# Optimization experiments

Measured on AMD Instinct MI355X. Metric: run time of the kernel, lower is better.

The kernel has to match this reference:

```python
import math
import jax, jax.numpy as jnp
import numpy as np

S, B, H = 2048, 1, 4096
NH, HD = 32, 128          # heads, head dim
ROT = HD // 2             # rotary dim per 2D-RoPE half = 64


def rotate_half(x):
    x1, x2 = jnp.split(x, 2, axis=-1)
    return jnp.concatenate([-x2, x1], axis=-1)


def rope_tables(seq_len, dim, base=10000.0):
    inv_freq = 1.0 / (base ** (jnp.arange(0, dim, 2, dtype=jnp.float32) / dim))
    freqs = jnp.arange(seq_len, dtype=jnp.float32)[:, None] * inv_freq[None, :]
    emb = jnp.concatenate([freqs, freqs], axis=-1)  # [S, dim]
    return jnp.cos(emb), jnp.sin(emb)


def apply_rope(q, k, cos, sin, pos):
    # q,k: [S,B,NH,ROT]; pos: [S,B] -> gather cos/sin per token
    c = cos[pos][:, :, None, :]  # [S,B,1,ROT]
    s = sin[pos][:, :, None, :]
    return q * c + rotate_half(q) * s, k * c + rotate_half(k) * s


def setup_inputs() -> dict:
    key = jax.random.key(0)
    ks = jax.random.split(key, 5)
    hidden_states = jax.random.normal(ks[0], (S, B, H), dtype=jnp.float32)
    pos = jnp.arange(S, dtype=jnp.int64 if jax.config.jax_enable_x64 else jnp.int32)
    position_ids = jnp.stack([pos, pos])[None]  # [B=1, 2, S]
    attention_mask = jnp.triu(jnp.ones((S, S), dtype=bool), k=1)[None, None]  # True = masked
    scale = 0.02
    wqkv = jax.random.normal(ks[1], (3 * H, H), dtype=jnp.float32) * scale
    bqkv = jax.random.normal(ks[2], (3 * H,), dtype=jnp.float32) * scale
    wdense = jax.random.normal(ks[3], (H, H), dtype=jnp.float32) * scale
    bdense = jax.random.normal(ks[4], (H,), dtype=jnp.float32) * scale
    return {"hidden_states": hidden_states, "position_ids": position_ids,
            "attention_mask": attention_mask, "wqkv": wqkv, "bqkv": bqkv,
            "wdense": wdense, "bdense": bdense, "layer_id": 1}


def reference(hidden_states, position_ids, attention_mask, wqkv, bqkv, wdense, bdense, layer_id):
    s, b, h = hidden_states.shape
    # fused QKV projection: [S,B,NH,3*HD]
    mixed = (jnp.einsum('sbh,oh->sbo', hidden_states, wqkv) + bqkv).reshape(s, b, NH, 3 * HD)
    q, k, v = jnp.split(mixed, 3, axis=-1)  # each [S,B,NH,HD]

    # 2D RoPE: split head dim in half, rotate each half with its own position ids
    q1, q2 = jnp.split(q, 2, axis=-1)
    k1, k2 = jnp.split(k, 2, axis=-1)
    cos, sin = rope_tables(s, ROT)
    pos = position_ids[:, 0, :].T       # [S,B]
    block_pos = position_ids[:, 1, :].T  # [S,B]
    q1, k1 = apply_rope(q1, k1, cos, sin, pos)
    q2, k2 = apply_rope(q2, k2, cos, sin, block_pos)
    q = jnp.concatenate([q1, q2], axis=-1)
    k = jnp.concatenate([k1, k2], axis=-1)

    # layer-scaled attention (ChatGLM style)
    coeff = float(layer_id + 1)
    q = q / (math.sqrt(HD) * coeff)
    scores = jnp.einsum('sbhd,tbhd->bhst', q, k)  # [B,NH,S,S]
    scores = jnp.where(attention_mask, jnp.float32(-10000.0), scores)
    scores = scores.astype(jnp.float32) * coeff
    probs = jax.nn.softmax(scores, axis=-1).astype(q.dtype)
    context = jnp.einsum('bhst,tbhd->sbhd', probs, v).reshape(s, b, h)

    out = jnp.einsum('sbh,oh->sbo', context, wdense) + bdense
    return out
```

## Files before the change

kernel.cpp:

```cpp
#include <hip/hip_runtime.h>

typedef unsigned short u16;
typedef unsigned int u32;
typedef __attribute__((ext_vector_type(4))) float f32x4;
typedef __attribute__((ext_vector_type(16))) float f32x16;
typedef __attribute__((ext_vector_type(8))) short bf16x8;
typedef __attribute__((ext_vector_type(2))) unsigned int u32x2;

#define S_LEN 2048
#define NHEAD 32
#define HDD 128
#define HID 4096
#define N_QKV 12288
#define KDIM 4096
#define RS 12288

__device__ __forceinline__ u16 f2bf(float f) {
  u32 u = __builtin_bit_cast(u32, f);
  u = (u + 0x7FFFu + ((u >> 16) & 1u)) >> 16;
  return (u16)u;
}
__device__ __forceinline__ float bf2f(u16 h) {
  u32 u = ((u32)h) << 16;
  return __builtin_bit_cast(float, u);
}

__device__ __forceinline__ void gl2lds16(const void* g, void* l) {
  __builtin_amdgcn_global_load_lds(
      (const __attribute__((address_space(1))) u32*)g,
      (__attribute__((address_space(3))) u32*)l, 16, 0, 0);
}

#define FULL_BAR()                          \
  {                                         \
    asm volatile("" ::: "memory");          \
    __builtin_amdgcn_s_barrier();           \
    asm volatile("" ::: "memory");          \
  }

__global__ __launch_bounds__(256) void cvt3_kernel(const float* __restrict__ s0, u16* __restrict__ d0, int n0,
                                                   const float* __restrict__ s2, u16* __restrict__ d2, int n2,
                                                   float* __restrict__ cos_t, float* __restrict__ sin_t) {
  int i = blockIdx.x * blockDim.x + threadIdx.x;
  if (i < S_LEN * 32) {
    int s = i >> 5, ii = i & 31;
    float invf = expf(-0.28782313662425572f * (float)ii);
    float a = (float)s * invf;
    cos_t[i] = cosf(a);
    sin_t[i] = sinf(a);
  }
  int st = gridDim.x * blockDim.x;
  int ntot = n0 + n2;
  for (; i < ntot; i += st) {
    const float* s;
    u16* d;
    int j = i;
    if (j < n0) {
      s = s0; d = d0;
    } else {
      j -= n0; s = s2; d = d2;
    }
    float4 v = ((const float4*)s)[j];
    u32x2 o;
    o.x = (u32)f2bf(v.x) | ((u32)f2bf(v.y) << 16);
    o.y = (u32)f2bf(v.z) | ((u32)f2bf(v.w) << 16);
    ((u32x2*)d)[j] = o;
  }
}

__global__ __launch_bounds__(256) void ropek_kernel(u16* __restrict__ mixed,
                                                    const int* __restrict__ pid,
                                                    const float* __restrict__ cos_t,
                                                    const float* __restrict__ sin_t) {
  int idx = blockIdx.x * blockDim.x + threadIdx.x;
  const int total = NHEAD * S_LEN * 2 * 8;
  if (idx >= total) return;
  int j = idx & 7;
  int half = (idx >> 3) & 1;
  int s = (idx >> 4) & (S_LEN - 1);
  int h = idx >> 15;
  int i0 = j * 4;
  int p = pid[half * S_LEN + s];
  float4 c4 = *(const float4*)(cos_t + p * 32 + i0);
  float4 s4 = *(const float4*)(sin_t + p * 32 + i0);
  u16* base = mixed + (size_t)s * RS + h * 384 + 128 + half * 64 + i0;
  ushort4 x1v = *(const ushort4*)(base);
  ushort4 x2v = *(const ushort4*)(base + 32);
  ushort4 o1, o2;
  {
    float x1 = bf2f(x1v.x), x2 = bf2f(x2v.x);
    o1.x = f2bf(x1 * c4.x - x2 * s4.x);
    o2.x = f2bf(x2 * c4.x + x1 * s4.x);
  }
  {
    float x1 = bf2f(x1v.y), x2 = bf2f(x2v.y);
    o1.y = f2bf(x1 * c4.y - x2 * s4.y);
    o2.y = f2bf(x2 * c4.y + x1 * s4.y);
  }
  {
    float x1 = bf2f(x1v.z), x2 = bf2f(x2v.z);
    o1.z = f2bf(x1 * c4.z - x2 * s4.z);
    o2.z = f2bf(x2 * c4.z + x1 * s4.z);
  }
  {
    float x1 = bf2f(x1v.w), x2 = bf2f(x2v.w);
    o1.w = f2bf(x1 * c4.w - x2 * s4.w);
    o2.w = f2bf(x2 * c4.w + x1 * s4.w);
  }
  *(ushort4*)(base) = o1;
  *(ushort4*)(base + 32) = o2;
}

__global__ __launch_bounds__(512, 2) void gemmQ(const u16* __restrict__ A,
                                                const u16* __restrict__ B,
                                                const float* __restrict__ bias,
                                                u16* __restrict__ outb) {
  __shared__ __align__(16) char lds[3][40960];

  const int tid = threadIdx.x;
  const int lane = tid & 63, w = tid >> 6;
  const int l31 = lane & 31, hh = lane >> 5;
  const int wm = w >> 2, wn = w & 3;

  int x = blockIdx.x & 7, loc = blockIdx.x >> 3;
  int mb = loc & 7, nb = x * 4 + (loc >> 3);
  const int bm = mb * 256, bn = nb * 384;

  f32x16 acc[4][3];
#pragma unroll
  for (int mi = 0; mi < 4; ++mi)
#pragma unroll
    for (int ni = 0; ni < 3; ++ni)
#pragma unroll
      for (int r = 0; r < 16; ++r) acc[mi][ni][r] = 0.f;

  const size_t K2 = (size_t)KDIM * 2;

  const char* gA[2];
#pragma unroll
  for (int j = 0; j < 2; ++j) {
    int slot = j * 512 + tid;
    int line = slot >> 3;
    int sl = (slot & 7) ^ (line & 7);
    int row = 2 * line + (sl >> 2);
    int colb = (sl & 3) * 16;
    gA[j] = (const char*)A + (size_t)(bm + row) * K2 + colb;
  }
  const char* gB[3];
#pragma unroll
  for (int j = 0; j < 3; ++j) {
    int slot = j * 512 + tid;
    int line = slot >> 3;
    int sl = (slot & 7) ^ (line & 7);
    int row = 2 * line + (sl >> 2);
    int colb = (sl & 3) * 16;
    gB[j] = (const char*)B + (size_t)(bn + row) * K2 + colb;
  }
  const int ldst = w * 1024;

#define QIA(t, bi)                                                  \
  {                                                                 \
    char* Lb = lds[bi];                                             \
    gl2lds16(gA[0] + (size_t)(t) * 64, Lb + ldst);                  \
    gl2lds16(gA[1] + (size_t)(t) * 64, Lb + 8192 + ldst);           \
  }
#define QIB(t, bi)                                                  \
  {                                                                 \
    char* Lb = lds[bi] + 16384;                                     \
    _Pragma("unroll")                                               \
    for (int j = 0; j < 3; ++j)                                     \
      gl2lds16(gB[j] + (size_t)(t) * 64, Lb + j * 8192 + ldst);     \
  }

  int offA[4][2], offB[3][2];
#pragma unroll
  for (int mi = 0; mi < 4; ++mi) {
    int r = wm * 128 + mi * 32 + l31;
    int line = r >> 1;
#pragma unroll
    for (int kk = 0; kk < 2; ++kk) {
      int sl = (((r & 1) << 2) + kk * 2 + hh) ^ (line & 7);
      offA[mi][kk] = line * 128 + sl * 16;
    }
  }
#pragma unroll
  for (int ni = 0; ni < 3; ++ni) {
    int r = wn * 96 + ni * 32 + l31;
    int line = r >> 1;
#pragma unroll
    for (int kk = 0; kk < 2; ++kk) {
      int sl = (((r & 1) << 2) + kk * 2 + hh) ^ (line & 7);
      offB[ni][kk] = 16384 + line * 128 + sl * 16;
    }
  }

  QIA(0, 0); QIB(0, 0);
  QIA(1, 1); QIB(1, 1);
  asm volatile("s_waitcnt vmcnt(5)" ::: "memory");
  FULL_BAR();

  int cur = 0, nx2 = 2;
  for (int kt = 0; kt < 128; ++kt) {
    const char* buf = lds[cur];
    const bool pf = (kt + 2) < 128;
    bf16x8 a[4], b[3];
#pragma unroll
    for (int mi = 0; mi < 4; ++mi) a[mi] = *(const bf16x8*)(buf + offA[mi][0]);
#pragma unroll
    for (int ni = 0; ni < 3; ++ni) b[ni] = *(const bf16x8*)(buf + offB[ni][0]);
    if (pf) QIA(kt + 2, nx2);
    FULL_BAR();
    __builtin_amdgcn_s_setprio(1);
#pragma unroll
    for (int mi = 0; mi < 4; ++mi)
#pragma unroll
      for (int ni = 0; ni < 3; ++ni)
        acc[mi][ni] = __builtin_amdgcn_mfma_f32_32x32x16_bf16(a[mi], b[ni], acc[mi][ni], 0, 0, 0);
    __builtin_amdgcn_s_setprio(0);
#pragma unroll
    for (int mi = 0; mi < 4; ++mi) a[mi] = *(const bf16x8*)(buf + offA[mi][1]);
#pragma unroll
    for (int ni = 0; ni < 3; ++ni) b[ni] = *(const bf16x8*)(buf + offB[ni][1]);
    if (pf) {
      QIB(kt + 2, nx2);
      asm volatile("s_waitcnt vmcnt(5)" ::: "memory");
    } else if (kt == 126) {
      asm volatile("s_waitcnt vmcnt(0)" ::: "memory");
    }
    FULL_BAR();
    __builtin_amdgcn_s_setprio(1);
#pragma unroll
    for (int mi = 0; mi < 4; ++mi)
#pragma unroll
      for (int ni = 0; ni < 3; ++ni)
        acc[mi][ni] = __builtin_amdgcn_mfma_f32_32x32x16_bf16(a[mi], b[ni], acc[mi][ni], 0, 0, 0);
    __builtin_amdgcn_s_setprio(0);
    cur = (cur + 1 == 3) ? 0 : cur + 1;
    nx2 = (nx2 + 1 == 3) ? 0 : nx2 + 1;
  }
#undef QIA
#undef QIB

#pragma unroll
  for (int ni = 0; ni < 3; ++ni) {
    int n = bn + wn * 96 + ni * 32 + l31;
    float bv = bias[n];
#pragma unroll
    for (int mi = 0; mi < 4; ++mi) {
      int m0 = bm + wm * 128 + mi * 32 + 4 * hh;
#pragma unroll
      for (int reg = 0; reg < 16; ++reg) {
        int row = m0 + (reg & 3) + 8 * (reg >> 2);
        outb[(size_t)row * N_QKV + n] = f2bf(acc[mi][ni][reg] + bv);
      }
    }
  }
}

__global__ __launch_bounds__(512, 2) void gemmD(const u16* __restrict__ A,
                                                const float* __restrict__ Bf,
                                                const float* __restrict__ bias,
                                                float* __restrict__ outf) {
  __shared__ __align__(16) char lds[2][49152];

  const int tid = threadIdx.x;
  const int lane = tid & 63, w = tid >> 6;
  const int l15 = lane & 15, g = lane >> 4;
  const int wm = w >> 1, wn = w & 1;

  int x = blockIdx.x & 7, loc = blockIdx.x >> 3;
  int mb = loc & 7, nb = x * 4 + (loc >> 3);
  const int bm = mb * 256, bn = nb * 128;

  f32x4 acc[4][4];
  f32x4 z4 = {0.f, 0.f, 0.f, 0.f};
#pragma unroll
  for (int mi = 0; mi < 4; ++mi)
#pragma unroll
    for (int ni = 0; ni < 4; ++ni) acc[mi][ni] = z4;

  const size_t K2 = (size_t)KDIM * 2;

  const char* gA[2];
#pragma unroll
  for (int j = 0; j < 2; ++j) {
    int slot = j * 512 + tid;
    int line = slot >> 3;
    int sl = (slot & 7) ^ (line & 7);
    int row = 2 * line + (sl >> 2);
    int colb = (sl & 3) * 16;
    gA[j] = (const char*)A + (size_t)(bm + row) * K2 + colb;
  }
  int bline = tid >> 3;
  int bsl = tid & 7;
  int brow = 2 * bline + (bsl >> 2);
  int bcole = (bsl & 3) * 8;
  const float* gBs = Bf + (size_t)(bn + brow) * KDIM + bcole;
  int bphys = bsl ^ (bline & 7);
  const int bwr = 32768 + bline * 128 + bphys * 16;
  const int ldst = w * 1024;

#define DIA(t, kk)                                                            \
  {                                                                           \
    char* Lb = lds[(t) & 1] + (kk) * 16384;                                   \
    gl2lds16(gA[0] + (size_t)(t) * 128 + (kk) * 64, Lb + ldst);               \
    gl2lds16(gA[1] + (size_t)(t) * 128 + (kk) * 64, Lb + 8192 + ldst);        \
  }
#define DGB(t)                                                                \
  {                                                                           \
    const float* p0 = gBs + (size_t)(t) * 64;                                 \
    b0a = *(const float4*)(p0);                                               \
    b0b = *(const float4*)(p0 + 4);                                           \
    b1a = *(const float4*)(p0 + 32);                                          \
    b1b = *(const float4*)(p0 + 36);                                          \
  }
#define DWB(t)                                                                \
  {                                                                           \
    bf16x8 o0, o1;                                                            \
    o0[0] = (short)f2bf(b0a.x); o0[1] = (short)f2bf(b0a.y);                   \
    o0[2] = (short)f2bf(b0a.z); o0[3] = (short)f2bf(b0a.w);                   \
    o0[4] = (short)f2bf(b0b.x); o0[5] = (short)f2bf(b0b.y);                   \
    o0[6] = (short)f2bf(b0b.z); o0[7] = (short)f2bf(b0b.w);                   \
    o1[0] = (short)f2bf(b1a.x); o1[1] = (short)f2bf(b1a.y);                   \
    o1[2] = (short)f2bf(b1a.z); o1[3] = (short)f2bf(b1a.w);                   \
    o1[4] = (short)f2bf(b1b.x); o1[5] = (short)f2bf(b1b.y);                   \
    o1[6] = (short)f2bf(b1b.z); o1[7] = (short)f2bf(b1b.w);                   \
    char* Lb = lds[(t) & 1];                                                  \
    *(bf16x8*)(Lb + bwr) = o0;                                                \
    *(bf16x8*)(Lb + 8192 + bwr) = o1;                                         \
  }

  int offA[4], offB[2][4];
#pragma unroll
  for (int mi = 0; mi < 4; ++mi) {
    int r = wm * 64 + mi * 16 + l15;
    int line = r >> 1;
    int sl = (((r & 1) << 2) + g) ^ (line & 7);
    offA[mi] = line * 128 + sl * 16;
  }
#pragma unroll
  for (int kk = 0; kk < 2; ++kk)
#pragma unroll
    for (int ni = 0; ni < 4; ++ni) {
      int r = wn * 64 + ni * 16 + l15;
      int line = r >> 1;
      int sl = (((r & 1) << 2) + g) ^ (line & 7);
      offB[kk][ni] = 32768 + kk * 8192 + line * 128 + sl * 16;
    }

  float4 b0a, b0b, b1a, b1b;
  DGB(0);
  DIA(0, 0);
  DIA(0, 1);
  asm volatile("s_waitcnt vmcnt(4)" ::: "memory");
  DWB(0);
  asm volatile("s_waitcnt vmcnt(0) lgkmcnt(0)" ::: "memory");
  FULL_BAR();

  for (int kt = 0; kt < 64; ++kt) {
    const char* buf = lds[kt & 1];
    const bool pf = (kt + 1) < 64;
    bf16x8 a[4], b[4];
#pragma unroll
    for (int mi = 0; mi < 4; ++mi) a[mi] = *(const bf16x8*)(buf + offA[mi]);
#pragma unroll
    for (int ni = 0; ni < 4; ++ni) b[ni] = *(const bf16x8*)(buf + offB[0][ni]);
    if (pf) {
      DIA(kt + 1, 0);
      DGB(kt + 1);
      asm volatile("s_waitcnt vmcnt(6)" ::: "memory");
    } else {
      asm volatile("s_waitcnt vmcnt(0)" ::: "memory");
    }
    FULL_BAR();
    __builtin_amdgcn_s_setprio(1);
#pragma unroll
    for (int mi = 0; mi < 4; ++mi)
#pragma unroll
      for (int ni = 0; ni < 4; ++ni)
        acc[mi][ni] = __builtin_amdgcn_mfma_f32_16x16x32_bf16(a[mi], b[ni], acc[mi][ni], 0, 0, 0);
    __builtin_amdgcn_s_setprio(0);
#pragma unroll
    for (int mi = 0; mi < 4; ++mi) a[mi] = *(const bf16x8*)(buf + 16384 + offA[mi]);
#pragma unroll
    for (int ni = 0; ni < 4; ++ni) b[ni] = *(const bf16x8*)(buf + offB[1][ni]);
    if (pf) {
      DIA(kt + 1, 1);
      asm volatile("s_waitcnt vmcnt(2)" ::: "memory");
      DWB(kt + 1);
      asm volatile("s_waitcnt lgkmcnt(0)" ::: "memory");
    }
    FULL_BAR();
    __builtin_amdgcn_s_setprio(1);
#pragma unroll
    for (int mi = 0; mi < 4; ++mi)
#pragma unroll
      for (int ni = 0; ni < 4; ++ni)
        acc[mi][ni] = __builtin_amdgcn_mfma_f32_16x16x32_bf16(a[mi], b[ni], acc[mi][ni], 0, 0, 0);
    __builtin_amdgcn_s_setprio(0);
  }
#undef DIA
#undef DGB
#undef DWB

#pragma unroll
  for (int ni = 0; ni < 4; ++ni) {
    int n = bn + wn * 64 + ni * 16 + l15;
    float bv = bias[n];
#pragma unroll
    for (int mi = 0; mi < 4; ++mi) {
      int m0 = bm + wm * 64 + mi * 16 + 4 * g;
#pragma unroll
      for (int rr = 0; rr < 4; ++rr) outf[(size_t)(m0 + rr) * HID + n] = acc[mi][ni][rr] + bv;
    }
  }
}

__global__ __launch_bounds__(256) void attn_kernel(const u16* __restrict__ mixed,
                                                   const int* __restrict__ pid,
                                                   const float* __restrict__ cos_t,
                                                   const float* __restrict__ sin_t,
                                                   u16* __restrict__ ctx) {
  __shared__ __align__(16) u16 Ksh[64 * 136];
  __shared__ __align__(16) u16 Vsh[128 * 64];
  __shared__ __align__(16) u16 Pt[4][16 * 72];

  int tid = threadIdx.x;
  int lane = tid & 63, w = tid >> 6;
  int lane15 = lane & 15, g = lane >> 4;

  int bpair = blockIdx.x & 15;
  int h = blockIdx.x >> 4;

  const u16* qp = mixed + (size_t)h * 384;
  const u16* kp = mixed + (size_t)h * 384 + 128;
  const u16* vp = mixed + (size_t)h * 384 + 256;

  int krow = tid >> 2, kc = (tid & 3) * 32;
  int vk0 = 2 * (tid & 31), vd0 = (tid >> 5) * 16;
  f32x4 z4 = {0.f, 0.f, 0.f, 0.f};
  const float QSC = 0.08838834764831845f;
  const float L2E = 1.4426950408889634f;

  for (int pass = 0; pass < 2; ++pass) {
    int qi = pass ? (31 - bpair) : bpair;
    int qbase = qi * 64;
    int qrow = qbase + w * 16 + lane15;
    int ntiles = qi + 1;

    bf16x8 qf[4];
    const u16* qptr = qp + (size_t)qrow * RS + g * 8;
#pragma unroll
    for (int d0 = 0; d0 < 4; ++d0) qf[d0] = *(const bf16x8*)(qptr + d0 * 32);
    {
      int p1 = pid[qrow], p2 = pid[S_LEN + qrow];
      float cc[8], ss[8], dd[8], tt[8];
#pragma unroll
      for (int j = 0; j < 8; ++j) {
        cc[j] = cos_t[p1 * 32 + g * 8 + j];
        ss[j] = sin_t[p1 * 32 + g * 8 + j];
        dd[j] = cos_t[p2 * 32 + g * 8 + j];
        tt[j] = sin_t[p2 * 32 + g * 8 + j];
      }
#pragma unroll
      for (int j = 0; j < 8; ++j) {
        float x1 = bf2f((u16)qf[0][j]), x2 = bf2f((u16)qf[1][j]);
        qf[0][j] = (short)f2bf((x1 * cc[j] - x2 * ss[j]) * QSC);
        qf[1][j] = (short)f2bf((x2 * cc[j] + x1 * ss[j]) * QSC);
        float y1 = bf2f((u16)qf[2][j]), y2 = bf2f((u16)qf[3][j]);
        qf[2][j] = (short)f2bf((y1 * dd[j] - y2 * tt[j]) * QSC);
        qf[3][j] = (short)f2bf((y2 * dd[j] + y1 * tt[j]) * QSC);
      }
    }

    f32x4 pv[8];
#pragma unroll
    for (int db = 0; db < 8; ++db) pv[db] = z4;
    float m_run = -1e30f, l_run = 0.0f;

    for (int t = 0; t < ntiles; ++t) {
      int kb0 = t * 64;
      __syncthreads();
      {
        const bf16x8* src = (const bf16x8*)(kp + (size_t)(kb0 + krow) * RS + kc);
#pragma unroll
        for (int c = 0; c < 4; ++c)
          *(bf16x8*)(Ksh + krow * 136 + kc + c * 8) = src[c];
        const bf16x8* r0p = (const bf16x8*)(vp + (size_t)(kb0 + vk0) * RS + vd0);
        const bf16x8* r1p = (const bf16x8*)(vp + (size_t)(kb0 + vk0 + 1) * RS + vd0);
        bf16x8 r00 = r0p[0], r01 = r0p[1];
        bf16x8 r10 = r1p[0], r11 = r1p[1];
#pragma unroll
        for (int jj = 0; jj < 8; ++jj) {
          int d = vd0 + jj;
          u32 v0 = (u32)(u16)r00[jj] | ((u32)(u16)r10[jj] << 16);
          *(u32*)((char*)Vsh + d * 128 + (((vk0 >> 3) ^ (d & 7)) << 4) + (vk0 & 7) * 2) = v0;
          int d2 = vd0 + 8 + jj;
          u32 v1 = (u32)(u16)r01[jj] | ((u32)(u16)r11[jj] << 16);
          *(u32*)((char*)Vsh + d2 * 128 + (((vk0 >> 3) ^ (d2 & 7)) << 4) + (vk0 & 7) * 2) = v1;
        }
      }
      __syncthreads();

      f32x4 sa[4];
#pragma unroll
      for (int kt16 = 0; kt16 < 4; ++kt16) sa[kt16] = z4;
#pragma unroll
      for (int kt16 = 0; kt16 < 4; ++kt16)
#pragma unroll
        for (int d0 = 0; d0 < 4; ++d0) {
          bf16x8 kf = *(const bf16x8*)(Ksh + (kt16 * 16 + lane15) * 136 + d0 * 32 + g * 8);
          sa[kt16] = __builtin_amdgcn_mfma_f32_16x16x32_bf16(kf, qf[d0], sa[kt16], 0, 0, 0);
        }
      float s[16];
#pragma unroll
      for (int kt16 = 0; kt16 < 4; ++kt16)
#pragma unroll
        for (int rr = 0; rr < 4; ++rr) {
          int kg = kb0 + kt16 * 16 + 4 * g + rr;
          s[kt16 * 4 + rr] = (kg > qrow) ? -1e30f : sa[kt16][rr];
        }
      float mx = s[0];
#pragma unroll
      for (int i2 = 1; i2 < 16; ++i2) mx = fmaxf(mx, s[i2]);
      mx = fmaxf(mx, __shfl_xor(mx, 16));
      mx = fmaxf(mx, __shfl_xor(mx, 32));
      float mnew = fmaxf(m_run, mx);
      float fac = exp2f((m_run - mnew) * L2E);
      float p[16], psum = 0.f;
#pragma unroll
      for (int i2 = 0; i2 < 16; ++i2) {
        p[i2] = exp2f((s[i2] - mnew) * L2E);
        psum += p[i2];
      }
      psum += __shfl_xor(psum, 16);
      psum += __shfl_xor(psum, 32);
      l_run = l_run * fac + psum;
      m_run = mnew;
#pragma unroll
      for (int db = 0; db < 8; ++db) pv[db] *= fac;

#pragma unroll
      for (int kt16 = 0; kt16 < 4; ++kt16) {
        u32x2 pw;
        pw.x = (u32)f2bf(p[kt16 * 4 + 0]) | ((u32)f2bf(p[kt16 * 4 + 1]) << 16);
        pw.y = (u32)f2bf(p[kt16 * 4 + 2]) | ((u32)f2bf(p[kt16 * 4 + 3]) << 16);
        *(u32x2*)(&Pt[w][lane15 * 72 + kt16 * 16 + 4 * g]) = pw;
      }
      asm volatile("s_waitcnt lgkmcnt(0)" ::: "memory");
      bf16x8 pf0 = *(const bf16x8*)(&Pt[w][lane15 * 72 + 8 * g]);
      bf16x8 pf1 = *(const bf16x8*)(&Pt[w][lane15 * 72 + 32 + 8 * g]);

#pragma unroll
      for (int db = 0; db < 8; ++db) {
        int d = db * 16 + lane15;
        bf16x8 vf0 = *(const bf16x8*)((const char*)Vsh + d * 128 + ((g ^ (d & 7)) << 4));
        bf16x8 vf1 = *(const bf16x8*)((const char*)Vsh + d * 128 + (((4 + g) ^ (d & 7)) << 4));
        pv[db] = __builtin_amdgcn_mfma_f32_16x16x32_bf16(vf0, pf0, pv[db], 0, 0, 0);
        pv[db] = __builtin_amdgcn_mfma_f32_16x16x32_bf16(vf1, pf1, pv[db], 0, 0, 0);
      }
    }

    float inv = 1.0f / l_run;
#pragma unroll
    for (int db = 0; db < 8; ++db) {
      ushort4 o;
      o.x = f2bf(pv[db][0] * inv);
      o.y = f2bf(pv[db][1] * inv);
      o.z = f2bf(pv[db][2] * inv);
      o.w = f2bf(pv[db][3] * inv);
      *(ushort4*)(ctx + (size_t)qrow * HID + h * HDD + db * 16 + 4 * g) = o;
    }
    __syncthreads();
  }
}

extern "C" void kernel_launch(void* const* d_in, const int* in_sizes, int n_in,
                              void* d_out, int out_size, void* d_ws, size_t ws_size,
                              hipStream_t stream) {
  const float* hidden = (const float*)d_in[0];
  const int* pid = (const int*)d_in[1];
  const float* wqkv = (const float*)d_in[3];
  const float* bqkv = (const float*)d_in[4];
  const float* wdense = (const float*)d_in[5];
  const float* bdense = (const float*)d_in[6];
  float* out = (float*)d_out;

  char* ws = (char*)d_ws;
  u16* W1 = (u16*)ws;
  u16* X = (u16*)(ws + 134217728);
  u16* mixed = (u16*)(ws + 150994944);
  u16* ctx = (u16*)(ws + 201326592);
  float* cos_t = (float*)(ws + 218103808);
  float* sin_t = (float*)(ws + 218365952);

  cvt3_kernel<<<dim3(2048), dim3(256), 0, stream>>>(
      wqkv, W1, N_QKV * KDIM / 4, hidden, X, S_LEN * HID / 4, cos_t, sin_t);

  gemmQ<<<dim3(256), dim3(512), 0, stream>>>(X, W1, bqkv, mixed);

  ropek_kernel<<<dim3(4096), dim3(256), 0, stream>>>(mixed, pid, cos_t, sin_t);

  attn_kernel<<<dim3(512), dim3(256), 0, stream>>>(mixed, pid, cos_t, sin_t, ctx);

  gemmD<<<dim3(256), dim3(512), 0, stream>>>(ctx, wdense, bdense, out);
}
```

Measured before the change: 484.9 us.

## Switch dense-projection GEMM to 32x32x16 MFMA and change LDS swizzle key

The output-projection GEMM now uses 32x32x16 bf16 MFMA tiles (2x2 per wave) instead of 16x16x32 (4x4 per wave), with LDS fragment offsets and the epilogue row mapping rewritten to match. The LDS XOR swizzle key in both GEMMs changes from line&7 to (line^(line>>1))&7, aiming to cut bank conflicts on the fragment reads. Larger MFMA tiles mean fewer instructions and fewer LDS reads per flop, but they carry different latency and register pressure, and the swizzle change alters the global-to-LDS load address pattern.

```diff
diff --git a/kernel.cpp b/kernel.cpp
--- a/kernel.cpp
+++ b/kernel.cpp
@@ -24,6 +24,8 @@
   u32 u = ((u32)h) << 16;
   return __builtin_bit_cast(float, u);
 }
+
+__device__ __forceinline__ int gkey(int line) { return (line ^ (line >> 1)) & 7; }
 
 __device__ __forceinline__ void gl2lds16(const void* g, void* l) {
   __builtin_amdgcn_global_load_lds(
@@ -141,7 +143,7 @@
   for (int j = 0; j < 2; ++j) {
     int slot = j * 512 + tid;
     int line = slot >> 3;
-    int sl = (slot & 7) ^ (line & 7);
+    int sl = (slot & 7) ^ gkey(line);
     int row = 2 * line + (sl >> 2);
     int colb = (sl & 3) * 16;
     gA[j] = (const char*)A + (size_t)(bm + row) * K2 + colb;
@@ -151,7 +153,7 @@
   for (int j = 0; j < 3; ++j) {
     int slot = j * 512 + tid;
     int line = slot >> 3;
-    int sl = (slot & 7) ^ (line & 7);
+    int sl = (slot & 7) ^ gkey(line);
     int row = 2 * line + (sl >> 2);
     int colb = (sl & 3) * 16;
     gB[j] = (const char*)B + (size_t)(bn + row) * K2 + colb;
@@ -179,7 +181,7 @@
     int line = r >> 1;
 #pragma unroll
     for (int kk = 0; kk < 2; ++kk) {
-      int sl = (((r & 1) << 2) + kk * 2 + hh) ^ (line & 7);
+      int sl = (((r & 1) << 2) + kk * 2 + hh) ^ gkey(line);
       offA[mi][kk] = line * 128 + sl * 16;
     }
   }
@@ -189,7 +191,7 @@
     int line = r >> 1;
 #pragma unroll
     for (int kk = 0; kk < 2; ++kk) {
-      int sl = (((r & 1) << 2) + kk * 2 + hh) ^ (line & 7);
+      int sl = (((r & 1) << 2) + kk * 2 + hh) ^ gkey(line);
       offB[ni][kk] = 16384 + line * 128 + sl * 16;
     }
   }
@@ -265,19 +267,20 @@
 
   const int tid = threadIdx.x;
   const int lane = tid & 63, w = tid >> 6;
-  const int l15 = lane & 15, g = lane >> 4;
+  const int l31 = lane & 31, hh = lane >> 5;
   const int wm = w >> 1, wn = w & 1;
 
   int x = blockIdx.x & 7, loc = blockIdx.x >> 3;
   int mb = loc & 7, nb = x * 4 + (loc >> 3);
   const int bm = mb * 256, bn = nb * 128;
 
-  f32x4 acc[4][4];
-  f32x4 z4 = {0.f, 0.f, 0.f, 0.f};
-#pragma unroll
-  for (int mi = 0; mi < 4; ++mi)
-#pragma unroll
-    for (int ni = 0; ni < 4; ++ni) acc[mi][ni] = z4;
+  f32x16 acc[2][2];
+#pragma unroll
+  for (int mi = 0; mi < 2; ++mi)
+#pragma unroll
+    for (int ni = 0; ni < 2; ++ni)
+#pragma unroll
+      for (int r = 0; r < 16; ++r) acc[mi][ni][r] = 0.f;
 
   const size_t K2 = (size_t)KDIM * 2;
 
@@ -286,7 +289,7 @@
   for (int j = 0; j < 2; ++j) {
     int slot = j * 512 + tid;
     int line = slot >> 3;
-    int sl = (slot & 7) ^ (line & 7);
+    int sl = (slot & 7) ^ gkey(line);
     int row = 2 * line + (sl >> 2);
     int colb = (sl & 3) * 16;
     gA[j] = (const char*)A + (size_t)(bm + row) * K2 + colb;
@@ -296,7 +299,7 @@
   int brow = 2 * bline + (bsl >> 2);
   int bcole = (bsl & 3) * 8;
   const float* gBs = Bf + (size_t)(bn + brow) * KDIM + bcole;
-  int bphys = bsl ^ (bline & 7);
+  int bphys = bsl ^ gkey(bline);
   const int bwr = 32768 + bline * 128 + bphys * 16;
   const int ldst = w * 1024;
 
@@ -330,23 +333,31 @@
     *(bf16x8*)(Lb + 8192 + bwr) = o1;                                         \
   }
 
-  int offA[4], offB[2][4];
-#pragma unroll
-  for (int mi = 0; mi < 4; ++mi) {
-    int r = wm * 64 + mi * 16 + l15;
+  int offA[2][2][2], offB[2][2][2];
+#pragma unroll
+  for (int mi = 0; mi < 2; ++mi) {
+    int r = wm * 64 + mi * 32 + l31;
     int line = r >> 1;
-    int sl = (((r & 1) << 2) + g) ^ (line & 7);
-    offA[mi] = line * 128 + sl * 16;
-  }
-#pragma unroll
-  for (int kk = 0; kk < 2; ++kk)
-#pragma unroll
-    for (int ni = 0; ni < 4; ++ni) {
-      int r = wn * 64 + ni * 16 + l15;
-      int line = r >> 1;
-      int sl = (((r & 1) << 2) + g) ^ (line & 7);
-      offB[kk][ni] = 32768 + kk * 8192 + line * 128 + sl * 16;
-    }
+#pragma unroll
+    for (int kku = 0; kku < 2; ++kku)
+#pragma unroll
+      for (int st = 0; st < 2; ++st) {
+        int sl = (((r & 1) << 2) + st * 2 + hh) ^ gkey(line);
+        offA[mi][kku][st] = kku * 16384 + line * 128 + sl * 16;
+      }
+  }
+#pragma unroll
+  for (int ni = 0; ni < 2; ++ni) {
+    int r = wn * 64 + ni * 32 + l31;
+    int line = r >> 1;
+#pragma unroll
+    for (int kku = 0; kku < 2; ++kku)
+#pragma unroll
+      for (int st = 0; st < 2; ++st) {
+        int sl = (((r & 1) << 2) + st * 2 + hh) ^ gkey(line);
+        offB[ni][kku][st] = 32768 + kku * 8192 + line * 128 + sl * 16;
+      }
+  }
 
   float4 b0a, b0b, b1a, b1b;
   DGB(0);
@@ -360,11 +371,15 @@
   for (int kt = 0; kt < 64; ++kt) {
     const char* buf = lds[kt & 1];
     const bool pf = (kt + 1) < 64;
-    bf16x8 a[4], b[4];
-#pragma unroll
-    for (int mi = 0; mi < 4; ++mi) a[mi] = *(const bf16x8*)(buf + offA[mi]);
-#pragma unroll
-    for (int ni = 0; ni < 4; ++ni) b[ni] = *(const bf16x8*)(buf + offB[0][ni]);
+    bf16x8 a[2][2], b[2][2];
+#pragma unroll
+    for (int mi = 0; mi < 2; ++mi)
+#pragma unroll
+      for (int st = 0; st < 2; ++st) a[mi][st] = *(const bf16x8*)(buf + offA[mi][0][st]);
+#pragma unroll
+    for (int ni = 0; ni < 2; ++ni)
+#pragma unroll
+      for (int st = 0; st < 2; ++st) b[ni][st] = *(const bf16x8*)(buf + offB[ni][0][st]);
     if (pf) {
       DIA(kt + 1, 0);
       DGB(kt + 1);
@@ -375,15 +390,21 @@
     FULL_BAR();
     __builtin_amdgcn_s_setprio(1);
 #pragma unroll
-    for (int mi = 0; mi < 4; ++mi)
-#pragma unroll
-      for (int ni = 0; ni < 4; ++ni)
-        acc[mi][ni] = __builtin_amdgcn_mfma_f32_16x16x32_bf16(a[mi], b[ni], acc[mi][ni], 0, 0, 0);
+    for (int st = 0; st < 2; ++st)
+#pragma unroll
+      for (int mi = 0; mi < 2; ++mi)
+#pragma unroll
+        for (int ni = 0; ni < 2; ++ni)
+          acc[mi][ni] = __builtin_amdgcn_mfma_f32_32x32x16_bf16(a[mi][st], b[ni][st], acc[mi][ni], 0, 0, 0);
     __builtin_amdgcn_s_setprio(0);
 #pragma unroll
-    for (int mi = 0; mi < 4; ++mi) a[mi] = *(const bf16x8*)(buf + 16384 + offA[mi]);
-#pragma unroll
-    for (int ni = 0; ni < 4; ++ni) b[ni] = *(const bf16x8*)(buf + offB[1][ni]);
+    for (int mi = 0; mi < 2; ++mi)
+#pragma unroll
+      for (int st = 0; st < 2; ++st) a[mi][st] = *(const bf16x8*)(buf + offA[mi][1][st]);
+#pragma unroll
+    for (int ni = 0; ni < 2; ++ni)
+#pragma unroll
+      for (int st = 0; st < 2; ++st) b[ni][st] = *(const bf16x8*)(buf + offB[ni][1][st]);
     if (pf) {
       DIA(kt + 1, 1);
       asm volatile("s_waitcnt vmcnt(2)" ::: "memory");
@@ -393,10 +414,12 @@
     FULL_BAR();
     __builtin_amdgcn_s_setprio(1);
 #pragma unroll
-    for (int mi = 0; mi < 4; ++mi)
-#pragma unroll
-      for (int ni = 0; ni < 4; ++ni)
-        acc[mi][ni] = __builtin_amdgcn_mfma_f32_16x16x32_bf16(a[mi], b[ni], acc[mi][ni], 0, 0, 0);
+    for (int st = 0; st < 2; ++st)
+#pragma unroll
+      for (int mi = 0; mi < 2; ++mi)
+#pragma unroll
+        for (int ni = 0; ni < 2; ++ni)
+          acc[mi][ni] = __builtin_amdgcn_mfma_f32_32x32x16_bf16(a[mi][st], b[ni][st], acc[mi][ni], 0, 0, 0);
     __builtin_amdgcn_s_setprio(0);
   }
 #undef DIA
@@ -404,14 +427,17 @@
 #undef DWB
 
 #pragma unroll
-  for (int ni = 0; ni < 4; ++ni) {
-    int n = bn + wn * 64 + ni * 16 + l15;
+  for (int ni = 0; ni < 2; ++ni) {
+    int n = bn + wn * 64 + ni * 32 + l31;
     float bv = bias[n];
 #pragma unroll
-    for (int mi = 0; mi < 4; ++mi) {
-      int m0 = bm + wm * 64 + mi * 16 + 4 * g;
-#pragma unroll
-      for (int rr = 0; rr < 4; ++rr) outf[(size_t)(m0 + rr) * HID + n] = acc[mi][ni][rr] + bv;
+    for (int mi = 0; mi < 2; ++mi) {
+      int m0 = bm + wm * 64 + mi * 32 + 4 * hh;
+#pragma unroll
+      for (int reg = 0; reg < 16; ++reg) {
+        int row = m0 + (reg & 3) + 8 * (reg >> 2);
+        outf[(size_t)row * HID + n] = acc[mi][ni][reg] + bv;
+      }
     }
   }
 }
```

New measurement: 483.1 us. No clear change (-0.4%).
